# Kernel tuning notes

Hardware: AMD Instinct MI355X
Metric: run time of the kernel (lower is better)

## Reference

```python
import jax, jax.numpy as jnp
import numpy as np

D_MODEL, D_FF, H, B, S = 1024, 4096, 16, 4, 2048
D_K = D_MODEL // H
EPS = 1e-5
NEG = -1e9


def _custom_ln(x, alpha, bias):
    # torch: mean, std (unbiased, N-1), alpha*(x-mean)/(std+eps)+bias; alpha/bias scalars
    mean = jnp.mean(x, axis=-1, keepdims=True)
    n = x.shape[-1]
    var = jnp.sum((x - mean) ** 2, axis=-1, keepdims=True) / (n - 1)
    std = jnp.sqrt(var)
    return alpha * (x - mean) / (std + EPS) + bias


def setup_inputs() -> dict:
    key = jax.random.key(0)
    ks = jax.random.split(key, 12)
    sc_d = 1.0 / np.sqrt(D_MODEL)
    sc_f = 1.0 / np.sqrt(D_FF)
    inp = {
        "x": jax.random.normal(ks[0], (B, S, D_MODEL), jnp.float32),
        "src_mask": jnp.ones((B, 1, 1, S), jnp.int32),
        "wq": jax.random.normal(ks[1], (D_MODEL, D_MODEL), jnp.float32) * sc_d,
        "bq": jnp.zeros((D_MODEL,), jnp.float32),
        "wk": jax.random.normal(ks[2], (D_MODEL, D_MODEL), jnp.float32) * sc_d,
        "bk": jnp.zeros((D_MODEL,), jnp.float32),
        "wv": jax.random.normal(ks[3], (D_MODEL, D_MODEL), jnp.float32) * sc_d,
        "bv": jnp.zeros((D_MODEL,), jnp.float32),
        "wo": jax.random.normal(ks[4], (D_MODEL, D_MODEL), jnp.float32) * sc_d,
        "bo": jnp.zeros((D_MODEL,), jnp.float32),
        "w1": jax.random.normal(ks[5], (D_MODEL, D_FF), jnp.float32) * sc_d,
        "b1": jnp.zeros((D_FF,), jnp.float32),
        "w2": jax.random.normal(ks[6], (D_FF, D_MODEL), jnp.float32) * sc_f,
        "b2": jnp.zeros((D_MODEL,), jnp.float32),
        "ln1_a": jnp.ones((1,), jnp.float32),
        "ln1_b": jnp.zeros((1,), jnp.float32),
        "ln2_a": jnp.ones((1,), jnp.float32),
        "ln2_b": jnp.zeros((1,), jnp.float32),
    }
    return inp


def _attention(xn, src_mask, wq, bq, wk, bk, wv, bv, wo, bo):
    q = (xn @ wq + bq).reshape(B, S, H, D_K).transpose(0, 2, 1, 3)  # [B,H,S,Dk]
    k = (xn @ wk + bk).reshape(B, S, H, D_K).transpose(0, 2, 1, 3)
    v = (xn @ wv + bv).reshape(B, S, H, D_K).transpose(0, 2, 1, 3)
    scores = jnp.einsum("bhqd,bhkd->bhqk", q, k) / np.sqrt(D_K)
    scores = jnp.where(src_mask == 0, NEG, scores)
    attn = jax.nn.softmax(scores, axis=-1)
    ctx = jnp.einsum("bhqk,bhkd->bhqd", attn, v)
    ctx = ctx.transpose(0, 2, 1, 3).reshape(B, S, D_MODEL)
    return ctx @ wo + bo


def reference(x, src_mask, wq, bq, wk, bk, wv, bv, wo, bo,
              w1, b1, w2, b2, ln1_a, ln1_b, ln2_a, ln2_b):
    # pre-LN attention residual (dropout=0 -> identity)
    xn = _custom_ln(x, ln1_a, ln1_b)
    x = x + _attention(xn, src_mask, wq, bq, wk, bk, wv, bv, wo, bo)
    # pre-LN FFN residual
    xn = _custom_ln(x, ln2_a, ln2_b)
    ff = jax.nn.relu(xn @ w1 + b1) @ w2 + b2
    return x + ff
```

## Files before the change

kernel.cpp:

```cpp
#include <hip/hip_runtime.h>

typedef unsigned short u16;
typedef __bf16 bf16x8 __attribute__((ext_vector_type(8)));
typedef float f32x4 __attribute__((ext_vector_type(4)));

__device__ __forceinline__ u16 f2bf(float f) {
  unsigned u = __builtin_bit_cast(unsigned, f);
  unsigned lsb = (u >> 16) & 1u;
  u += 0x7fffu + lsb;
  return (u16)(u >> 16);
}

__device__ __forceinline__ unsigned cvt_pk_bf16(float lo, float hi) {
  unsigned r;
  asm("v_cvt_pk_bf16_f32 %0, %1, %2" : "=v"(r) : "v"(lo), "v"(hi));
  return r;
}

__device__ __forceinline__ void gld_lds16(const u16* g, u16* l) {
  __builtin_amdgcn_global_load_lds(
      (__attribute__((address_space(1))) void*)g,
      (__attribute__((address_space(3))) void*)l, 16, 0, 0);
}

__global__ __launch_bounds__(256) void ln_kernel(
    const float* __restrict__ x, u16* __restrict__ out,
    const float* __restrict__ alpha_p, const float* __restrict__ beta_p) {
  const int row = blockIdx.x;
  const int t = threadIdx.x;
  const float4 v = reinterpret_cast<const float4*>(x + (size_t)row * 1024)[t];
  float s = v.x + v.y + v.z + v.w;
  float sq = v.x * v.x + v.y * v.y + v.z * v.z + v.w * v.w;
#pragma unroll
  for (int off = 32; off > 0; off >>= 1) {
    s += __shfl_down(s, off);
    sq += __shfl_down(sq, off);
  }
  __shared__ float red[8];
  const int w = t >> 6;
  if ((t & 63) == 0) { red[w] = s; red[4 + w] = sq; }
  __syncthreads();
  const float ts = red[0] + red[1] + red[2] + red[3];
  const float tq = red[4] + red[5] + red[6] + red[7];
  const float mean = ts * (1.0f / 1024.0f);
  float var = (tq - ts * mean) * (1.0f / 1023.0f);
  var = fmaxf(var, 0.0f);
  const float rden = 1.0f / (sqrtf(var) + 1e-5f);
  const float a = alpha_p[0], bb = beta_p[0];
  uint2 ov;
  ov.x = cvt_pk_bf16(a * (v.x - mean) * rden + bb, a * (v.y - mean) * rden + bb);
  ov.y = cvt_pk_bf16(a * (v.z - mean) * rden + bb, a * (v.w - mean) * rden + bb);
  reinterpret_cast<uint2*>(out + (size_t)row * 1024)[t] = ov;
}

__global__ __launch_bounds__(256) void wcvt_t(
    const float* __restrict__ w, u16* __restrict__ wt, int K, int N, float scale) {
  __shared__ float tile[32][33];
  const int n0 = blockIdx.x * 32, k0 = blockIdx.y * 32;
  const int tx = threadIdx.x, ty = threadIdx.y;
#pragma unroll
  for (int i = 0; i < 4; ++i)
    tile[ty + i * 8][tx] = w[(size_t)(k0 + ty + i * 8) * N + n0 + tx];
  __syncthreads();
#pragma unroll
  for (int i = 0; i < 4; ++i)
    wt[(size_t)(n0 + ty + i * 8) * K + k0 + tx] = f2bf(tile[tx][ty + i * 8] * scale);
}

__global__ __launch_bounds__(256) void pack_bias(
    const float* __restrict__ a, const float* __restrict__ b,
    const float* __restrict__ c, float* __restrict__ o, float qscale) {
  const int i = blockIdx.x * 256 + threadIdx.x;
  o[i] = (i < 1024) ? a[i] * qscale : ((i < 2048) ? b[i - 1024] : c[i - 2048]);
}

__global__ __launch_bounds__(256) void mk_mbias(
    const int* __restrict__ mask, float* __restrict__ mb, int* __restrict__ flags) {
  const int b = blockIdx.x, t = threadIdx.x;
  __shared__ int bad;
  if (t == 0) bad = 0;
  __syncthreads();
  int loc = 0;
#pragma unroll
  for (int i = 0; i < 8; ++i) {
    const int idx = b * 2048 + t * 8 + i;
    const int mv = mask[idx];
    mb[idx] = mv ? 0.f : -1.4427e9f;
    loc |= (mv == 0);
  }
  if (loc) atomicOr(&bad, 1);
  __syncthreads();
  if (t == 0) flags[b] = !bad;
}

template <int EPI, int BM>
__global__ __launch_bounds__(256) void gemm_bt(
    const u16* __restrict__ A, const u16* __restrict__ Bt,
    const float* __restrict__ bias, const float* __restrict__ res,
    void* __restrict__ Cout, u16* __restrict__ vt, int M, int N, int K) {
  constexpr int MF = BM / 32;
  __shared__ u16 As[BM * 32];
  __shared__ u16 Bs[128 * 32];
  const int tid = threadIdx.x;
  const int l = tid & 63;
  const int w = tid >> 6;
  const int wr = w >> 1, wc = w & 1;
  const int gx = gridDim.x;
  int id = blockIdx.y * gx + blockIdx.x;
  const int nwg = gx * gridDim.y;
  id = (id & 7) * (nwg >> 3) + (id >> 3);
  const int n0 = (id % gx) * 128;
  const int m0 = (id / gx) * BM;
  const int lr = l & 15, lk = (l >> 4) * 8;

  f32x4 acc[MF][4];
#pragma unroll
  for (int i = 0; i < MF; ++i)
#pragma unroll
    for (int j = 0; j < 4; ++j) acc[i][j] = f32x4{0.f, 0.f, 0.f, 0.f};

  const int srow = tid >> 2;
  const int scol = (tid & 3) * 8;
  const u16* gA0 = A + (size_t)(m0 + srow) * K + scol;
  const u16* gA1 = A + (size_t)(m0 + 64 + srow) * K + scol;
  const u16* gB0 = Bt + (size_t)(n0 + srow) * K + scol;
  const u16* gB1 = Bt + (size_t)(n0 + 64 + srow) * K + scol;
  u16* lA0 = &As[tid * 8];
  u16* lA1 = &As[2048 + tid * 8];
  u16* lB0 = &Bs[tid * 8];
  u16* lB1 = &Bs[2048 + tid * 8];

  for (int k0 = 0; k0 < K; k0 += 32) {
    gld_lds16(gA0 + k0, lA0);
    if constexpr (BM == 128) gld_lds16(gA1 + k0, lA1);
    gld_lds16(gB0 + k0, lB0);
    gld_lds16(gB1 + k0, lB1);
    __syncthreads();
    bf16x8 a[MF], b[4];
#pragma unroll
    for (int mf = 0; mf < MF; ++mf)
      a[mf] = *reinterpret_cast<const bf16x8*>(&As[(wr * (BM / 2) + mf * 16 + lr) * 32 + lk]);
#pragma unroll
    for (int nf = 0; nf < 4; ++nf)
      b[nf] = *reinterpret_cast<const bf16x8*>(&Bs[(wc * 64 + nf * 16 + lr) * 32 + lk]);
#pragma unroll
    for (int mf = 0; mf < MF; ++mf)
#pragma unroll
      for (int nf = 0; nf < 4; ++nf)
        acc[mf][nf] = __builtin_amdgcn_mfma_f32_16x16x32_bf16(a[mf], b[nf], acc[mf][nf], 0, 0, 0);
    __syncthreads();
  }

  if (EPI == 3 && n0 >= 2048) {
#pragma unroll
    for (int mf = 0; mf < MF; ++mf) {
#pragma unroll
      for (int nf = 0; nf < 4; ++nf) {
        const int col = n0 + wc * 64 + nf * 16 + lr;
        const float bv = bias[col];
        const int row0 = m0 + wr * (BM / 2) + mf * 16 + (l >> 4) * 4;
        const int bb = row0 >> 11, s0 = row0 & 2047;
        const int d = col - 2048;
        uint2 pv;
        pv.x = cvt_pk_bf16(acc[mf][nf][0] + bv, acc[mf][nf][1] + bv);
        pv.y = cvt_pk_bf16(acc[mf][nf][2] + bv, acc[mf][nf][3] + bv);
        *reinterpret_cast<uint2*>(vt + ((size_t)bb * 1024 + d) * 2048 + s0) = pv;
      }
    }
    return;
  }

#pragma unroll
  for (int mf = 0; mf < MF; ++mf) {
#pragma unroll
    for (int nf = 0; nf < 4; ++nf) {
      const int col = n0 + wc * 64 + nf * 16 + lr;
      const float bv = bias[col];
#pragma unroll
      for (int j = 0; j < 4; ++j) {
        const int row = m0 + wr * (BM / 2) + mf * 16 + (l >> 4) * 4 + j;
        const size_t idx = (size_t)row * N + col;
        const float vv = acc[mf][nf][j] + bv;
        if (EPI == 0 || EPI == 3)
          ((u16*)Cout)[idx] = f2bf(vv);
        else if (EPI == 1)
          ((float*)Cout)[idx] = vv + res[idx];
        else
          ((u16*)Cout)[idx] = f2bf(fmaxf(vv, 0.f));
      }
    }
  }
}

__global__ __launch_bounds__(256, 4) void attn_fwd6(
    const u16* __restrict__ qkv, const u16* __restrict__ vt,
    const float* __restrict__ mbias, const int* __restrict__ flags,
    u16* __restrict__ ctx) {
  __shared__ u16 Ks[2][64 * 64];
  __shared__ u16 Vs[2][64 * 64];
  const int tid = threadIdx.x;
  const int l = tid & 63;
  const int w = tid >> 6;
  const int p = blockIdx.y * 16 + blockIdx.x;
  const int idx = p >> 3;
  const int bh = (p & 7) * 8 + (idx >> 4);
  const int qx = idx & 15;
  const int b = bh >> 4, h = bh & 15;
  const int r0 = qx * 128 + w * 32;
  const int lr = l & 15, lg = l >> 4;

  const u16* qb = qkv + (size_t)b * 2048 * 3072 + h * 64;
  const u16* kp = qb + 1024;
  const u16* vb = vt + ((size_t)b * 1024 + h * 64) * 2048;
  const float* mb = mbias + (size_t)b * 2048;
  const int allLive = flags[b];

  bf16x8 qf[2][2];
#pragma unroll
  for (int m = 0; m < 2; ++m)
#pragma unroll
    for (int ks = 0; ks < 2; ++ks)
      qf[m][ks] = *reinterpret_cast<const bf16x8*>(
          qb + (size_t)(r0 + m * 16 + lr) * 3072 + ks * 32 + lg * 8);

  float mrun[2] = {-1e30f, -1e30f};
  float lrun[2] = {0.f, 0.f};
  f32x4 o[2][4];
#pragma unroll
  for (int m = 0; m < 2; ++m)
#pragma unroll
    for (int d = 0; d < 4; ++d) o[m][d] = f32x4{0.f, 0.f, 0.f, 0.f};

  const u16* kS[2];
  const u16* vS[2];
#pragma unroll
  for (int i = 0; i < 2; ++i) {
    const int ci = tid + i * 256;
    const int row = ci >> 3, cc = ci & 7;
    const int sc = cc ^ (row & 7);
    kS[i] = kp + (size_t)row * 3072 + sc * 8;
    vS[i] = vb + (size_t)row * 2048 + sc * 8;
  }
#pragma unroll
  for (int i = 0; i < 2; ++i) {
    const int ci8 = (tid + i * 256) * 8;
    gld_lds16(kS[i], &Ks[0][ci8]);
    gld_lds16(vS[i], &Vs[0][ci8]);
  }
  asm volatile("s_waitcnt vmcnt(0)" ::: "memory");
  __syncthreads();

  union U8 { unsigned u[4]; bf16x8 v; };

  int cur = 0;
  for (int t = 0; t < 32; ++t) {
    const int kb0 = t * 64;
    if (t + 1 < 32) {
      const int nb = kb0 + 64;
#pragma unroll
      for (int i = 0; i < 2; ++i) {
        const int ci8 = (tid + i * 256) * 8;
        gld_lds16(kS[i] + (size_t)nb * 3072, &Ks[cur ^ 1][ci8]);
        gld_lds16(vS[i] + nb, &Vs[cur ^ 1][ci8]);
      }
    }

    f32x4 st[2][4];
    __builtin_amdgcn_s_setprio(1);
#pragma unroll
    for (int cf = 0; cf < 4; ++cf) {
      const int krow = cf * 16 + lr;
      const int ch0 = lg ^ (krow & 7);
      const int ch1 = (4 + lg) ^ (krow & 7);
      const bf16x8 kf0 = *reinterpret_cast<const bf16x8*>(&Ks[cur][krow * 64 + ch0 * 8]);
      const bf16x8 kf1 = *reinterpret_cast<const bf16x8*>(&Ks[cur][krow * 64 + ch1 * 8]);
#pragma unroll
      for (int m = 0; m < 2; ++m) {
        f32x4 acc = __builtin_amdgcn_mfma_f32_16x16x32_bf16(kf0, qf[m][0],
                                                            f32x4{0.f, 0.f, 0.f, 0.f}, 0, 0, 0);
        st[m][cf] = __builtin_amdgcn_mfma_f32_16x16x32_bf16(kf1, qf[m][1], acc, 0, 0, 0);
      }
    }
    __builtin_amdgcn_s_setprio(0);

    if (!allLive) {
#pragma unroll
      for (int cf = 0; cf < 4; ++cf) {
        const float4 m4 = *reinterpret_cast<const float4*>(mb + kb0 + cf * 16 + lg * 4);
#pragma unroll
        for (int m = 0; m < 2; ++m) {
          st[m][cf][0] += m4.x;
          st[m][cf][1] += m4.y;
          st[m][cf][2] += m4.z;
          st[m][cf][3] += m4.w;
        }
      }
    }

    bf16x8 paA[2], paB[2];
#pragma unroll
    for (int m = 0; m < 2; ++m) {
      float p0 = fmaxf(fmaxf(st[m][0][0], st[m][0][1]), st[m][0][2]);
      float p1 = fmaxf(fmaxf(st[m][0][3], st[m][1][0]), st[m][1][1]);
      float p2 = fmaxf(fmaxf(st[m][1][2], st[m][1][3]), st[m][2][0]);
      float p3 = fmaxf(fmaxf(st[m][2][1], st[m][2][2]), st[m][2][3]);
      float p4 = fmaxf(fmaxf(st[m][3][0], st[m][3][1]), st[m][3][2]);
      float pm = fmaxf(fmaxf(p0, p1), p2);
      pm = fmaxf(fmaxf(pm, p3), p4);
      pm = fmaxf(pm, st[m][3][3]);
      pm = fmaxf(pm, __shfl_xor(pm, 16));
      pm = fmaxf(pm, __shfl_xor(pm, 32));
      if (__any(pm > mrun[m] + 8.f)) {
        const float mn = fmaxf(mrun[m], pm);
        const float corr = exp2f(mrun[m] - mn);
        mrun[m] = mn;
        lrun[m] *= corr;
#pragma unroll
        for (int d = 0; d < 4; ++d)
#pragma unroll
          for (int j = 0; j < 4; ++j) o[m][d][j] *= corr;
      }
      float rs = 0.f;
#pragma unroll
      for (int cf = 0; cf < 4; ++cf)
#pragma unroll
        for (int j = 0; j < 4; ++j) {
          const float pp = exp2f(st[m][cf][j] - mrun[m]);
          st[m][cf][j] = pp;
          rs += pp;
        }
      rs += __shfl_xor(rs, 16);
      rs += __shfl_xor(rs, 32);
      lrun[m] += rs;

      unsigned pk[4][2];
#pragma unroll
      for (int cf = 0; cf < 4; ++cf)
#pragma unroll
        for (int wp = 0; wp < 2; ++wp)
          pk[cf][wp] = cvt_pk_bf16(st[m][cf][2 * wp], st[m][cf][2 * wp + 1]);

      U8 a0, a1;
#pragma unroll
      for (int c = 0; c < 2; ++c) {
        const int src = lr + 16 * ((2 * lg + c) & 3);
#pragma unroll
        for (int wp = 0; wp < 2; ++wp) {
          const int v00 = __shfl((int)pk[0][wp], src);
          const int v01 = __shfl((int)pk[1][wp], src);
          const int v10 = __shfl((int)pk[2][wp], src);
          const int v11 = __shfl((int)pk[3][wp], src);
          a0.u[2 * c + wp] = (unsigned)((lg < 2) ? v00 : v01);
          a1.u[2 * c + wp] = (unsigned)((lg < 2) ? v10 : v11);
        }
      }
      paA[m] = a0.v;
      paB[m] = a1.v;
    }

    __builtin_amdgcn_s_setprio(1);
#pragma unroll
    for (int df = 0; df < 4; ++df) {
      const int vrow = df * 16 + lr;
      const int ch0 = lg ^ (vrow & 7);
      const int ch1 = (4 + lg) ^ (vrow & 7);
      const bf16x8 vf0 = *reinterpret_cast<const bf16x8*>(&Vs[cur][vrow * 64 + ch0 * 8]);
      const bf16x8 vf1 = *reinterpret_cast<const bf16x8*>(&Vs[cur][vrow * 64 + ch1 * 8]);
#pragma unroll
      for (int m = 0; m < 2; ++m) {
        o[m][df] = __builtin_amdgcn_mfma_f32_16x16x32_bf16(vf0, paA[m], o[m][df], 0, 0, 0);
        o[m][df] = __builtin_amdgcn_mfma_f32_16x16x32_bf16(vf1, paB[m], o[m][df], 0, 0, 0);
      }
    }
    __builtin_amdgcn_s_setprio(0);

    asm volatile("s_waitcnt vmcnt(0)" ::: "memory");
    __syncthreads();
    cur ^= 1;
  }

#pragma unroll
  for (int m = 0; m < 2; ++m) {
    const float rdiv = 1.f / lrun[m];
    const size_t rowbase = ((size_t)b * 2048 + r0 + m * 16 + lr) * 1024 + h * 64;
#pragma unroll
    for (int df = 0; df < 4; ++df) {
      uint2 s4;
      s4.x = cvt_pk_bf16(o[m][df][0] * rdiv, o[m][df][1] * rdiv);
      s4.y = cvt_pk_bf16(o[m][df][2] * rdiv, o[m][df][3] * rdiv);
      *reinterpret_cast<uint2*>(ctx + rowbase + df * 16 + lg * 4) = s4;
    }
  }
}

extern "C" void kernel_launch(void* const* d_in, const int* in_sizes, int n_in,
                              void* d_out, int out_size, void* d_ws, size_t ws_size,
                              hipStream_t stream) {
  const float* x = (const float*)d_in[0];
  const int* mask = (const int*)d_in[1];
  const float* wq = (const float*)d_in[2];
  const float* bq = (const float*)d_in[3];
  const float* wk = (const float*)d_in[4];
  const float* bk = (const float*)d_in[5];
  const float* wv = (const float*)d_in[6];
  const float* bv = (const float*)d_in[7];
  const float* wo = (const float*)d_in[8];
  const float* bo = (const float*)d_in[9];
  const float* w1 = (const float*)d_in[10];
  const float* b1 = (const float*)d_in[11];
  const float* w2 = (const float*)d_in[12];
  const float* b2 = (const float*)d_in[13];
  const float* ln1a = (const float*)d_in[14];
  const float* ln1b = (const float*)d_in[15];
  const float* ln2a = (const float*)d_in[16];
  const float* ln2b = (const float*)d_in[17];

  const float SCL2 = 0.125f * 1.4426950408889634f;

  char* ws = (char*)d_ws;
  const size_t MB = 1024ull * 1024ull;
  u16* WTQKV = (u16*)(ws + 0 * MB);
  u16* WTO = (u16*)(ws + 6 * MB);
  u16* W1T = (u16*)(ws + 8 * MB);
  u16* W2T = (u16*)(ws + 16 * MB);
  float* BQKV = (float*)(ws + 24 * MB);
  float* MBIAS = (float*)(ws + 24 * MB + 65536);
  int* FLAGS = (int*)(ws + 24 * MB + 131072);
  u16* QKV = (u16*)(ws + 25 * MB);
  u16* VT = (u16*)(ws + 73 * MB);
  u16* XN = (u16*)(ws + 89 * MB);
  u16* CTX = (u16*)(ws + 105 * MB);
  float* X2 = (float*)(ws + 25 * MB);
  u16* XN2 = (u16*)(ws + 57 * MB);
  u16* H1 = (u16*)(ws + 73 * MB);

  dim3 bt(32, 8);
  wcvt_t<<<dim3(32, 32), bt, 0, stream>>>(wq, WTQKV, 1024, 1024, SCL2);
  wcvt_t<<<dim3(32, 32), bt, 0, stream>>>(wk, WTQKV + 1024 * 1024, 1024, 1024, 1.f);
  wcvt_t<<<dim3(32, 32), bt, 0, stream>>>(wv, WTQKV + 2048 * 1024, 1024, 1024, 1.f);
  wcvt_t<<<dim3(32, 32), bt, 0, stream>>>(wo, WTO, 1024, 1024, 1.f);
  wcvt_t<<<dim3(128, 32), bt, 0, stream>>>(w1, W1T, 1024, 4096, 1.f);
  wcvt_t<<<dim3(32, 128), bt, 0, stream>>>(w2, W2T, 4096, 1024, 1.f);
  pack_bias<<<dim3(12), 256, 0, stream>>>(bq, bk, bv, BQKV, SCL2);
  mk_mbias<<<dim3(4), 256, 0, stream>>>(mask, MBIAS, FLAGS);

  ln_kernel<<<8192, 256, 0, stream>>>(x, XN, ln1a, ln1b);
  gemm_bt<3, 128><<<dim3(24, 64), 256, 0, stream>>>(XN, WTQKV, BQKV, nullptr, QKV, VT, 8192, 3072, 1024);
  attn_fwd6<<<dim3(16, 64), 256, 0, stream>>>(QKV, VT, MBIAS, FLAGS, CTX);
  gemm_bt<1, 64><<<dim3(8, 128), 256, 0, stream>>>(CTX, WTO, bo, x, X2, nullptr, 8192, 1024, 1024);
  ln_kernel<<<8192, 256, 0, stream>>>(X2, XN2, ln2a, ln2b);
  gemm_bt<2, 128><<<dim3(32, 64), 256, 0, stream>>>(XN2, W1T, b1, nullptr, H1, nullptr, 8192, 4096, 1024);
  gemm_bt<1, 64><<<dim3(8, 128), 256, 0, stream>>>(H1, W2T, b2, X2, (float*)d_out, nullptr, 8192, 1024, 4096);
}
```

Before: 499.4 us.

## Double-buffer GEMM LDS loads and compute softmax row sums via MFMA

The GEMM main loop now double-buffers its A/B tiles in LDS, issuing the global-to-LDS loads for the next K step before running the MFMAs on the current one. This is meant to hide load latency behind compute, at the cost of twice the shared memory and possibly lower occupancy. Separately, the attention kernel drops the per-row exp sum reduction with cross-lane shuffles. It instead accumulates the row sums with extra MFMAs that multiply a ones vector by the bf16 probabilities. That frees VALU and shuffle work but sums the rounded bf16 values, which slightly changes the numerics.

```diff
diff --git a/kernel.cpp b/kernel.cpp
--- a/kernel.cpp
+++ b/kernel.cpp
@@ -99,8 +99,8 @@
     const float* __restrict__ bias, const float* __restrict__ res,
     void* __restrict__ Cout, u16* __restrict__ vt, int M, int N, int K) {
   constexpr int MF = BM / 32;
-  __shared__ u16 As[BM * 32];
-  __shared__ u16 Bs[128 * 32];
+  __shared__ u16 As[2][BM * 32];
+  __shared__ u16 Bs[2][128 * 32];
   const int tid = threadIdx.x;
   const int l = tid & 63;
   const int w = tid >> 6;
@@ -125,30 +125,38 @@
   const u16* gA1 = A + (size_t)(m0 + 64 + srow) * K + scol;
   const u16* gB0 = Bt + (size_t)(n0 + srow) * K + scol;
   const u16* gB1 = Bt + (size_t)(n0 + 64 + srow) * K + scol;
-  u16* lA0 = &As[tid * 8];
-  u16* lA1 = &As[2048 + tid * 8];
-  u16* lB0 = &Bs[tid * 8];
-  u16* lB1 = &Bs[2048 + tid * 8];
-
+
+  gld_lds16(gA0, &As[0][tid * 8]);
+  if constexpr (BM == 128) gld_lds16(gA1, &As[0][2048 + tid * 8]);
+  gld_lds16(gB0, &Bs[0][tid * 8]);
+  gld_lds16(gB1, &Bs[0][2048 + tid * 8]);
+  asm volatile("s_waitcnt vmcnt(0)" ::: "memory");
+  __syncthreads();
+
+  int cur = 0;
   for (int k0 = 0; k0 < K; k0 += 32) {
-    gld_lds16(gA0 + k0, lA0);
-    if constexpr (BM == 128) gld_lds16(gA1 + k0, lA1);
-    gld_lds16(gB0 + k0, lB0);
-    gld_lds16(gB1 + k0, lB1);
-    __syncthreads();
+    if (k0 + 32 < K) {
+      const int kn = k0 + 32;
+      gld_lds16(gA0 + kn, &As[cur ^ 1][tid * 8]);
+      if constexpr (BM == 128) gld_lds16(gA1 + kn, &As[cur ^ 1][2048 + tid * 8]);
+      gld_lds16(gB0 + kn, &Bs[cur ^ 1][tid * 8]);
+      gld_lds16(gB1 + kn, &Bs[cur ^ 1][2048 + tid * 8]);
+    }
     bf16x8 a[MF], b[4];
 #pragma unroll
     for (int mf = 0; mf < MF; ++mf)
-      a[mf] = *reinterpret_cast<const bf16x8*>(&As[(wr * (BM / 2) + mf * 16 + lr) * 32 + lk]);
+      a[mf] = *reinterpret_cast<const bf16x8*>(&As[cur][(wr * (BM / 2) + mf * 16 + lr) * 32 + lk]);
 #pragma unroll
     for (int nf = 0; nf < 4; ++nf)
-      b[nf] = *reinterpret_cast<const bf16x8*>(&Bs[(wc * 64 + nf * 16 + lr) * 32 + lk]);
+      b[nf] = *reinterpret_cast<const bf16x8*>(&Bs[cur][(wc * 64 + nf * 16 + lr) * 32 + lk]);
 #pragma unroll
     for (int mf = 0; mf < MF; ++mf)
 #pragma unroll
       for (int nf = 0; nf < 4; ++nf)
         acc[mf][nf] = __builtin_amdgcn_mfma_f32_16x16x32_bf16(a[mf], b[nf], acc[mf][nf], 0, 0, 0);
+    asm volatile("s_waitcnt vmcnt(0)" ::: "memory");
     __syncthreads();
+    cur ^= 1;
   }
 
   if (EPI == 3 && n0 >= 2048) {
@@ -192,7 +200,7 @@
   }
 }
 
-__global__ __launch_bounds__(256, 4) void attn_fwd6(
+__global__ __launch_bounds__(256, 4) void attn_fwd7(
     const u16* __restrict__ qkv, const u16* __restrict__ vt,
     const float* __restrict__ mbias, const int* __restrict__ flags,
     u16* __restrict__ ctx) {
@@ -223,13 +231,19 @@
       qf[m][ks] = *reinterpret_cast<const bf16x8*>(
           qb + (size_t)(r0 + m * 16 + lr) * 3072 + ks * 32 + lg * 8);
 
+  bf16x8 ones;
+#pragma unroll
+  for (int e = 0; e < 8; ++e) ones[e] = (__bf16)1.0f;
+
   float mrun[2] = {-1e30f, -1e30f};
-  float lrun[2] = {0.f, 0.f};
+  f32x4 osum[2];
   f32x4 o[2][4];
 #pragma unroll
-  for (int m = 0; m < 2; ++m)
+  for (int m = 0; m < 2; ++m) {
+    osum[m] = f32x4{0.f, 0.f, 0.f, 0.f};
 #pragma unroll
     for (int d = 0; d < 4; ++d) o[m][d] = f32x4{0.f, 0.f, 0.f, 0.f};
+  }
 
   const u16* kS[2];
   const u16* vS[2];
@@ -314,24 +328,18 @@
         const float mn = fmaxf(mrun[m], pm);
         const float corr = exp2f(mrun[m] - mn);
         mrun[m] = mn;
-        lrun[m] *= corr;
+#pragma unroll
+        for (int j = 0; j < 4; ++j) osum[m][j] *= corr;
 #pragma unroll
         for (int d = 0; d < 4; ++d)
 #pragma unroll
           for (int j = 0; j < 4; ++j) o[m][d][j] *= corr;
       }
-      float rs = 0.f;
 #pragma unroll
       for (int cf = 0; cf < 4; ++cf)
 #pragma unroll
-        for (int j = 0; j < 4; ++j) {
-          const float pp = exp2f(st[m][cf][j] - mrun[m]);
-          st[m][cf][j] = pp;
-          rs += pp;
-        }
-      rs += __shfl_xor(rs, 16);
-      rs += __shfl_xor(rs, 32);
-      lrun[m] += rs;
+        for (int j = 0; j < 4; ++j)
+          st[m][cf][j] = exp2f(st[m][cf][j] - mrun[m]);
 
       unsigned pk[4][2];
 #pragma unroll
@@ -372,6 +380,11 @@
         o[m][df] = __builtin_amdgcn_mfma_f32_16x16x32_bf16(vf1, paB[m], o[m][df], 0, 0, 0);
       }
     }
+#pragma unroll
+    for (int m = 0; m < 2; ++m) {
+      osum[m] = __builtin_amdgcn_mfma_f32_16x16x32_bf16(ones, paA[m], osum[m], 0, 0, 0);
+      osum[m] = __builtin_amdgcn_mfma_f32_16x16x32_bf16(ones, paB[m], osum[m], 0, 0, 0);
+    }
     __builtin_amdgcn_s_setprio(0);
 
     asm volatile("s_waitcnt vmcnt(0)" ::: "memory");
@@ -381,7 +394,7 @@
 
 #pragma unroll
   for (int m = 0; m < 2; ++m) {
-    const float rdiv = 1.f / lrun[m];
+    const float rdiv = 1.f / osum[m][0];
     const size_t rowbase = ((size_t)b * 2048 + r0 + m * 16 + lr) * 1024 + h * 64;
 #pragma unroll
     for (int df = 0; df < 4; ++df) {
@@ -446,7 +459,7 @@
 
   ln_kernel<<<8192, 256, 0, stream>>>(x, XN, ln1a, ln1b);
   gemm_bt<3, 128><<<dim3(24, 64), 256, 0, stream>>>(XN, WTQKV, BQKV, nullptr, QKV, VT, 8192, 3072, 1024);
-  attn_fwd6<<<dim3(16, 64), 256, 0, stream>>>(QKV, VT, MBIAS, FLAGS, CTX);
+  attn_fwd7<<<dim3(16, 64), 256, 0, stream>>>(QKV, VT, MBIAS, FLAGS, CTX);
   gemm_bt<1, 64><<<dim3(8, 128), 256, 0, stream>>>(CTX, WTO, bo, x, X2, nullptr, 8192, 1024, 1024);
   ln_kernel<<<8192, 256, 0, stream>>>(X2, XN2, ln2a, ln2b);
   gemm_bt<2, 128><<<dim3(32, 64), 256, 0, stream>>>(XN2, W1T, b1, nullptr, H1, nullptr, 8192, 4096, 1024);
```

Result: faster. 486.9 us (-2.5%).
